# Kernel tuning notes

Measured on AMD Instinct MI355X. Metric: run time of the kernel, lower is better.

The kernel has to match this reference:

```python
import jax, jax.numpy as jnp
import numpy as np

B, N, DIM = 4, 2048, 128
HEADS, HEAD = 8, 128
INNER = HEADS * HEAD  # 1024
EPS = 1e-5


def setup_inputs() -> dict:
    key = jax.random.key(0)
    k0, k1, k2 = jax.random.split(key, 3)
    return {
        "x": jax.random.normal(k0, (B, N, DIM), jnp.float32),
        "ln_gamma": jnp.ones((DIM,), jnp.float32),
        "ln_beta": jnp.zeros((DIM,), jnp.float32),
        "w_qkv": jax.random.normal(k1, (3 * INNER, DIM), jnp.float32) * (DIM ** -0.5),
        "w_out": jax.random.normal(k2, (DIM, INNER), jnp.float32) * (INNER ** -0.5),
        "b_out": jnp.zeros((DIM,), jnp.float32),
    }


def _rope(t):
    """lucidrains-style rotary embedding over full last dim of t: [b,h,n,d]."""
    n, d = t.shape[-2], t.shape[-1]
    inv_freq = 1.0 / (10000.0 ** (jnp.arange(0, d, 2, dtype=jnp.float32) / d))
    freqs = jnp.arange(n, dtype=jnp.float32)[:, None] * inv_freq[None, :]  # [n, d/2]
    freqs = jnp.repeat(freqs, 2, axis=-1)  # interleaved duplicate -> [n, d]
    cos, sin = jnp.cos(freqs), jnp.sin(freqs)
    # rotate_half on interleaved pairs: (x1, x2) -> (-x2, x1)
    x1, x2 = t[..., 0::2], t[..., 1::2]
    rot = jnp.stack((-x2, x1), axis=-1).reshape(t.shape)
    return t * cos + rot * sin


def reference(x, ln_gamma, ln_beta, w_qkv, w_out, b_out):
    # LayerNorm
    mu = x.mean(-1, keepdims=True)
    var = x.var(-1, keepdims=True)
    xn = (x - mu) * jax.lax.rsqrt(var + EPS) * ln_gamma + ln_beta
    # QKV projection (bias-free)
    qkv = jnp.einsum('bnd,ed->bne', xn, w_qkv)  # [B, N, 3*INNER]
    q, k, v = jnp.split(qkv, 3, axis=-1)
    to_heads = lambda t: t.reshape(B, N, HEADS, HEAD).transpose(0, 2, 1, 3)
    q, k, v = to_heads(q), to_heads(k), to_heads(v)  # [B, H, N, HEAD]
    # Partial RoPE: rotate all but the last token; last token stays unrotated
    q = jnp.concatenate([_rope(q[:, :, :-1]), q[:, :, -1:]], axis=2)
    k = jnp.concatenate([_rope(k[:, :, :-1]), k[:, :, -1:]], axis=2)
    scale = HEAD ** -0.5
    dots = jnp.einsum('bhid,bhjd->bhij', q, k) * scale  # [B, H, N, N]
    attn = jax.nn.softmax(dots, axis=-1)
    out = jnp.einsum('bhij,bhjd->bhid', attn, v)
    out = out.transpose(0, 2, 1, 3).reshape(B, N, INNER)
    return out @ w_out.T + b_out
```

## Files before the change

kernel.cpp:

```cpp
#include <hip/hip_runtime.h>
#include <hip/hip_bf16.h>
#include <hip/hip_fp16.h>

#define B_      4
#define N_      2048
#define DIM_    128
#define HEADS_  8
#define HEAD_   128
#define INNER_  1024
#define QKV_    3072
#define EPS_    1e-5f
#define SCALE_  0.08838834764831845f
#define ROPE_C  0.20762050593046015f

typedef __attribute__((ext_vector_type(8))) short short8;
typedef __attribute__((ext_vector_type(4))) short short4v;
typedef __attribute__((ext_vector_type(4))) float f32x4;
typedef __attribute__((ext_vector_type(16))) float f32x16;


__device__ __forceinline__ unsigned short f2bf(float f) {
    unsigned u = __builtin_bit_cast(unsigned, f);
    u = (u + 0x7fffu + ((u >> 16) & 1u)) >> 16;
    return (unsigned short)u;
}
__device__ __forceinline__ float bf2f(unsigned short h) {
    unsigned u = ((unsigned)h) << 16;
    return __builtin_bit_cast(float, u);
}
__device__ __forceinline__ unsigned pk2(float a, float b) {
    return (unsigned)f2bf(a) | ((unsigned)f2bf(b) << 16);
}
__device__ __forceinline__ short4v pack4(const float* e) {
    __hip_bfloat162 h0 = __float22bfloat162_rn(make_float2(e[0], e[1]));
    __hip_bfloat162 h1 = __float22bfloat162_rn(make_float2(e[2], e[3]));
    uint2 u;
    __builtin_memcpy(&u.x, &h0, 4);
    __builtin_memcpy(&u.y, &h1, 4);
    return __builtin_bit_cast(short4v, u);
}

__global__ __launch_bounds__(256) void k_prep(
    const float* __restrict__ x, const float* __restrict__ g,
    const float* __restrict__ be, const float* __restrict__ w_qkv,
    const float* __restrict__ w_out, unsigned short* __restrict__ xnb,
    unsigned short* __restrict__ wqb, unsigned short* __restrict__ wob)
{
    const int bid = blockIdx.x;
    if (bid < 2048) {
        const int w = threadIdx.x >> 6, l = threadIdx.x & 63;
        const int row = bid * 4 + w;
        float2 v = *(const float2*)(x + (size_t)row * 128 + l * 2);
        float s = v.x + v.y, s2 = v.x * v.x + v.y * v.y;
#pragma unroll
        for (int off = 1; off < 64; off <<= 1) {
            s  += __shfl_xor(s, off);
            s2 += __shfl_xor(s2, off);
        }
        float mu = s * (1.f / 128.f);
        float var = s2 * (1.f / 128.f) - mu * mu;
        float rs = rsqrtf(var + EPS_);
        float2 gg = *(const float2*)(g + l * 2);
        float2 bb = *(const float2*)(be + l * 2);
        float ox = (v.x - mu) * rs * gg.x + bb.x;
        float oy = (v.y - mu) * rs * gg.y + bb.y;
        *(unsigned*)(xnb + (size_t)row * 128 + l * 2) = pk2(ox, oy);
    } else if (bid < 2240) {
        size_t i = ((size_t)(bid - 2048) * 256 + threadIdx.x) * 8;
        float4 f0 = *(const float4*)(w_qkv + i), f1 = *(const float4*)(w_qkv + i + 4);
        uint4 u = { pk2(f0.x, f0.y), pk2(f0.z, f0.w), pk2(f1.x, f1.y), pk2(f1.z, f1.w) };
        *(uint4*)(wqb + i) = u;
    } else {
        size_t i = ((size_t)(bid - 2240) * 256 + threadIdx.x) * 8;
        float4 f0 = *(const float4*)(w_out + i), f1 = *(const float4*)(w_out + i + 4);
        uint4 u = { pk2(f0.x, f0.y), pk2(f0.z, f0.w), pk2(f1.x, f1.y), pk2(f1.z, f1.w) };
        *(uint4*)(wob + i) = u;
    }
}

__global__ __launch_bounds__(256) void k_qkvf(
    const unsigned short* __restrict__ xnb, const unsigned short* __restrict__ wb,
    unsigned short* __restrict__ Q, unsigned short* __restrict__ K,
    unsigned short* __restrict__ Vt)
{
    __shared__ unsigned short lA[128 * 128];
    __shared__ unsigned short lB[128 * 128];
    const int t = threadIdx.x;
    const int wv = t >> 6, l = t & 63;
    const int lm = l & 15, quad = l >> 4;
    const int row0 = blockIdx.x * 128;
    const int by   = blockIdx.y;
    const int e0   = by * 128;

#pragma unroll
    for (int i = 0; i < 8; ++i) {
        int c = t + 256 * i;  int r = c >> 4, c8 = c & 15;
        int sc = (c8 ^ (r & 7)) * 8;
        *(uint4*)&lA[r * 128 + sc] =
            *(const uint4*)(xnb + (size_t)(row0 + r) * 128 + c8 * 8);
        *(uint4*)&lB[r * 128 + sc] =
            *(const uint4*)(wb + (size_t)(e0 + r) * 128 + c8 * 8);
    }
    __syncthreads();

    short8 af[2][4];
#pragma unroll
    for (int mt = 0; mt < 2; ++mt)
#pragma unroll
        for (int ks = 0; ks < 4; ++ks) {
            int r = wv * 32 + mt * 16 + lm;
            af[mt][ks] = *(short8*)&lA[r * 128 + (((ks * 4 + quad) ^ (r & 7)) << 3)];
        }

    f32x4 acc[2][8];
#pragma unroll
    for (int mt = 0; mt < 2; ++mt)
#pragma unroll
        for (int ct = 0; ct < 8; ++ct) acc[mt][ct] = (f32x4){0.f, 0.f, 0.f, 0.f};
#pragma unroll
    for (int ks = 0; ks < 4; ++ks) {
#pragma unroll
        for (int ct = 0; ct < 8; ++ct) {
            int r = ct * 16 + lm;
            short8 b = *(short8*)&lB[r * 128 + (((ks * 4 + quad) ^ (r & 7)) << 3)];
            acc[0][ct] = __builtin_amdgcn_mfma_f32_16x16x32_bf16(af[0][ks], b, acc[0][ct], 0, 0, 0);
            acc[1][ct] = __builtin_amdgcn_mfma_f32_16x16x32_bf16(af[1][ks], b, acc[1][ct], 0, 0, 0);
        }
    }
    __syncthreads();

    const int b  = row0 >> 11;
    const int n0 = row0 & (N_ - 1);
    const int h  = by & 7;
    const int bh = b * 8 + h;

    if (by < 16) {
#pragma unroll
        for (int mt = 0; mt < 2; ++mt)
#pragma unroll
            for (int ct = 0; ct < 8; ++ct)
#pragma unroll
                for (int r = 0; r < 4; ++r) {
                    int row = wv * 32 + mt * 16 + quad * 4 + r;
                    int chunk = ct * 2 + (lm >> 3);
                    lA[row * 128 + ((chunk ^ (row & 7)) << 3) + (lm & 7)] =
                        f2bf(acc[mt][ct][r]);
                }
        __syncthreads();

        const int r_loc = t >> 1, half = t & 1;
        const int n = n0 + r_loc;
        unsigned short* dst = (by < 8 ? Q : K) +
            ((size_t)bh * N_ + n) * HEAD_ + half * 64;
        const bool dorope = (n != N_ - 1);
#pragma unroll
        for (int j = 0; j < 8; ++j) {
            short8 vv = *(short8*)&lA[r_loc * 128 + (((half * 8 + j) ^ (r_loc & 7)) << 3)];
            if (dorope) {
                unsigned short* pv = (unsigned short*)&vv;
#pragma unroll
                for (int p = 0; p < 4; ++p) {
                    int i0 = half * 32 + j * 4 + p;
                    float invf = exp2f(-(float)i0 * ROPE_C);
                    float th = (float)n * invf;
                    float cs = __cosf(th), sn = __sinf(th);
                    float e = bf2f(pv[2 * p]), o = bf2f(pv[2 * p + 1]);
                    pv[2 * p]     = f2bf(e * cs - o * sn);
                    pv[2 * p + 1] = f2bf(o * cs + e * sn);
                }
            }
            *(short8*)(dst + j * 8) = vv;
        }
    } else {
#pragma unroll
        for (int mt = 0; mt < 2; ++mt)
#pragma unroll
            for (int ct = 0; ct < 8; ++ct)
#pragma unroll
                for (int r = 0; r < 4; ++r) {
                    int row = ct * 16 + lm;
                    int chunk = wv * 4 + mt * 2 + (quad & 1);
                    int off   = (quad >> 1) * 4 + r;
                    lA[row * 128 + ((chunk ^ (row & 7)) << 3) + off] =
                        f2bf(acc[mt][ct][r]);
                }
        __syncthreads();

        const int d = t >> 1, half = t & 1;
        unsigned short* dst = Vt + ((size_t)bh * HEAD_ + d) * N_ + n0 + half * 64;
#pragma unroll
        for (int j = 0; j < 8; ++j)
            *(short8*)(dst + j * 8) =
                *(short8*)&lA[d * 128 + (((half * 8 + j) ^ (d & 7)) << 3)];
    }
}

__global__ __launch_bounds__(256) void k_attn(
    const unsigned short* __restrict__ Q, const unsigned short* __restrict__ K,
    const unsigned short* __restrict__ Vt, unsigned short* __restrict__ Ob)
{
    __shared__ unsigned short lK[64 * 136];
    __shared__ unsigned short lV[128 * 72];

    const int t = threadIdx.x;
    const int w = t >> 6, l = t & 63;
    const int q32 = l & 31, hi = l >> 5;
    const int bid = blockIdx.x;
    const int bh = bid & 31;
    const int qt = bid >> 5;
    const int n0 = qt * 128;
    const unsigned short* Qb = Q  + (size_t)bh * N_ * HEAD_;
    const unsigned short* Kb = K  + (size_t)bh * N_ * HEAD_;
    const unsigned short* Vb = Vt + (size_t)bh * N_ * HEAD_;

    short8 aq[8];
    {
        const unsigned short* qp =
            Qb + (size_t)(n0 + w * 32 + q32) * 128 + hi * 8;
#pragma unroll
        for (int kc = 0; kc < 8; ++kc)
            aq[kc] = *(const short8*)(qp + kc * 16);
    }

    f32x16 Oa[4];
#pragma unroll
    for (int i = 0; i < 4; ++i)
        Oa[i] = (f32x16){0.f,0.f,0.f,0.f,0.f,0.f,0.f,0.f,
                         0.f,0.f,0.f,0.f,0.f,0.f,0.f,0.f};
    float ps = 0.f;
    const float C1 = SCALE_ * 1.44269504f;
    const float C0 = -23.08312f;

    short8 kr[4], vr[4];
#pragma unroll
    for (int i = 0; i < 4; ++i) {
        int c = t + 256 * i;
        kr[i] = *(const short8*)(Kb + ((size_t)(c >> 4)) * 128 + (c & 15) * 8);
        vr[i] = *(const short8*)(Vb + (size_t)(c >> 3) * N_ + (c & 7) * 8);
    }

    for (int jt = 0; jt < 32; ++jt) {
        __syncthreads();
#pragma unroll
        for (int i = 0; i < 4; ++i) {
            int c = t + 256 * i;
            *(short8*)&lK[(c >> 4) * 136 + (c & 15) * 8] = kr[i];
            *(short8*)&lV[(c >> 3) * 72  + (c & 7)  * 8] = vr[i];
        }
        __syncthreads();
        if (jt < 31) {
#pragma unroll
            for (int i = 0; i < 4; ++i) {
                int c = t + 256 * i;
                kr[i] = *(const short8*)(Kb + ((size_t)((jt + 1) * 64 + (c >> 4))) * 128 + (c & 15) * 8);
                vr[i] = *(const short8*)(Vb + (size_t)(c >> 3) * N_ + (jt + 1) * 64 + (c & 7) * 8);
            }
        }

        f32x16 st0 = (f32x16){0.f,0.f,0.f,0.f,0.f,0.f,0.f,0.f,
                              0.f,0.f,0.f,0.f,0.f,0.f,0.f,0.f};
        f32x16 st1 = st0;
#pragma unroll
        for (int kc = 0; kc < 8; ++kc) {
            short8 kf0 = *(short8*)&lK[q32 * 136 + kc * 16 + hi * 8];
            short8 kf1 = *(short8*)&lK[(32 + q32) * 136 + kc * 16 + hi * 8];
            st0 = __builtin_amdgcn_mfma_f32_32x32x16_bf16(kf0, aq[kc], st0, 0, 0, 0);
            st1 = __builtin_amdgcn_mfma_f32_32x32x16_bf16(kf1, aq[kc], st1, 0, 0, 0);
        }

        short8 pa[4];
#pragma unroll
        for (int T = 0; T < 2; ++T) {
#pragma unroll
            for (int g = 0; g < 2; ++g) {
                float e[8];
#pragma unroll
                for (int j = 0; j < 8; ++j) {
                    float s = T ? st1[8 * g + j] : st0[8 * g + j];
                    e[j] = exp2f(s * C1 + C0);
                    ps += e[j];
                }
                short4v lo = pack4(e);
                short4v hh = pack4(e + 4);
                pa[T * 2 + g] = __builtin_shufflevector(lo, hh, 0, 1, 2, 3, 4, 5, 6, 7);
            }
        }

#pragma unroll
        for (int dt = 0; dt < 4; ++dt) {
            const int d = dt * 32 + q32;
#pragma unroll
            for (int kc = 0; kc < 4; ++kc) {
                short8 bv = *(short8*)&lV[d * 72 + kc * 16 + hi * 8];
                Oa[dt] = __builtin_amdgcn_mfma_f32_32x32x16_bf16(pa[kc], bv, Oa[dt], 0, 0, 0);
            }
        }
    }

    ps += __shfl_xor(ps, 32);
    float inv = 1.f / ps;
    float ilq[16];
#pragma unroll
    for (int m = 0; m < 4; ++m)
#pragma unroll
        for (int r = 0; r < 4; ++r)
            ilq[m * 4 + r] = __shfl(inv, 4 * hi + r + 8 * m);

    const int b = bh >> 3, h = bh & 7;
#pragma unroll
    for (int dt = 0; dt < 4; ++dt) {
        const int d = dt * 32 + q32;
#pragma unroll
        for (int m = 0; m < 4; ++m)
#pragma unroll
            for (int r = 0; r < 4; ++r) {
                int q = 4 * hi + r + 8 * m;
                int n = n0 + w * 32 + q;
                Ob[((size_t)b * N_ + n) * INNER_ + h * HEAD_ + d] =
                    f2bf(Oa[dt][m * 4 + r] * ilq[m * 4 + r]);
            }
    }
}

__global__ __launch_bounds__(256) void k_proj(
    const unsigned short* __restrict__ Ob, const unsigned short* __restrict__ wob,
    const float* __restrict__ bias, float* __restrict__ out)
{
    __shared__ unsigned short lA[32 * 136];
    __shared__ unsigned short lB[64 * 136];
    float* lCf = (float*)lA;
    const int t = threadIdx.x;
    const int wv = t >> 6, l = t & 63;
    const int lm = l & 15, quad = l >> 4;
    const int rt = wv & 1, ch = wv >> 1;
    const int row0 = blockIdx.x * 32;
    const int e0   = blockIdx.y * 64;

    f32x4 acc[2];
#pragma unroll
    for (int ct = 0; ct < 2; ++ct) acc[ct] = (f32x4){0.f, 0.f, 0.f, 0.f};

    for (int kt = 0; kt < 8; ++kt) {
        __syncthreads();
#pragma unroll
        for (int i = 0; i < 2; ++i) {
            int c = t + 256 * i;  int r = c >> 4, c8 = c & 15;
            *(uint4*)&lA[r * 136 + c8 * 8] =
                *(const uint4*)(Ob + (size_t)(row0 + r) * 1024 + kt * 128 + c8 * 8);
        }
#pragma unroll
        for (int i = 0; i < 4; ++i) {
            int c = t + 256 * i;  int r = c >> 4, c8 = c & 15;
            *(uint4*)&lB[r * 136 + c8 * 8] =
                *(const uint4*)(wob + (size_t)(e0 + r) * 1024 + kt * 128 + c8 * 8);
        }
        __syncthreads();
        short8 a_[4];
#pragma unroll
        for (int ks = 0; ks < 4; ++ks)
            a_[ks] = *(short8*)&lA[(rt * 16 + lm) * 136 + ks * 32 + quad * 8];
#pragma unroll
        for (int ks = 0; ks < 4; ++ks)
#pragma unroll
            for (int ct = 0; ct < 2; ++ct) {
                short8 b = *(short8*)&lB[(ch * 32 + ct * 16 + lm) * 136 + ks * 32 + quad * 8];
                acc[ct] = __builtin_amdgcn_mfma_f32_16x16x32_bf16(a_[ks], b, acc[ct], 0, 0, 0);
            }
    }
    __syncthreads();
#pragma unroll
    for (int ct = 0; ct < 2; ++ct)
#pragma unroll
        for (int r = 0; r < 4; ++r)
            lCf[(rt * 16 + quad * 4 + r) * 68 + ch * 32 + ct * 16 + lm] = acc[ct][r];
    __syncthreads();
#pragma unroll
    for (int i = 0; i < 2; ++i) {
        int c = t + 256 * i;  int r = c >> 4, c4 = c & 15;
        float4 v = *(float4*)&lCf[r * 68 + c4 * 4];
        float4 b4 = *(const float4*)(bias + e0 + c4 * 4);
        v.x += b4.x; v.y += b4.y; v.z += b4.z; v.w += b4.w;
        *(float4*)(out + (size_t)(row0 + r) * 128 + e0 + c4 * 4) = v;
    }
}

extern "C" void kernel_launch(void* const* d_in, const int* in_sizes, int n_in,
                              void* d_out, int out_size, void* d_ws, size_t ws_size,
                              hipStream_t stream) {
    const float* x      = (const float*)d_in[0];
    const float* gamma  = (const float*)d_in[1];
    const float* beta   = (const float*)d_in[2];
    const float* w_qkv  = (const float*)d_in[3];
    const float* w_out  = (const float*)d_in[4];
    const float* b_out  = (const float*)d_in[5];
    float* out = (float*)d_out;
    char* wsb = (char*)d_ws;
    unsigned short* Q    = (unsigned short*)(wsb);
    unsigned short* K    = (unsigned short*)(wsb + (16ull << 20));
    unsigned short* Vt   = (unsigned short*)(wsb + (32ull << 20));
    unsigned short* Ob   = (unsigned short*)(wsb + (48ull << 20));
    unsigned short* xnb  = (unsigned short*)(wsb + (96ull << 20));
    unsigned short* wqb  = (unsigned short*)(wsb + (98ull << 20));
    unsigned short* wob  = (unsigned short*)(wsb + (99ull << 20));

    k_prep <<<dim3(2304),    256, 0, stream>>>(x, gamma, beta, w_qkv, w_out,
                                               xnb, wqb, wob);
    k_qkvf <<<dim3(64, 24),  256, 0, stream>>>(xnb, wqb, Q, K, Vt);
    k_attn <<<dim3(512),     256, 0, stream>>>(Q, K, Vt, Ob);
    k_proj <<<dim3(256, 2),  256, 0, stream>>>(Ob, wob, b_out, out);
}
```

Before: 191.2 us.

## Fuse output projection into attention kernel via per-head atomic accumulation

Removes the separate projection kernel and the bf16 intermediate attention-output buffer. Each attention block stages its normalized output tile in shared memory, multiplies it by the matching head slice of the output weight using MFMA, and atomically adds the partial sums into the fp32 output. The prep kernel now initializes the output with the bias. This saves one launch plus a global write and read of the intermediate, but adds 8-way atomic contention per output element and makes the summation order nondeterministic.

```diff
diff --git a/kernel.cpp b/kernel.cpp
--- a/kernel.cpp
+++ b/kernel.cpp
@@ -43,8 +43,9 @@
 __global__ __launch_bounds__(256) void k_prep(
     const float* __restrict__ x, const float* __restrict__ g,
     const float* __restrict__ be, const float* __restrict__ w_qkv,
-    const float* __restrict__ w_out, unsigned short* __restrict__ xnb,
-    unsigned short* __restrict__ wqb, unsigned short* __restrict__ wob)
+    const float* __restrict__ w_out, const float* __restrict__ bias,
+    unsigned short* __restrict__ xnb, unsigned short* __restrict__ wqb,
+    unsigned short* __restrict__ wob, float* __restrict__ out)
 {
     const int bid = blockIdx.x;
     if (bid < 2048) {
@@ -70,11 +71,15 @@
         float4 f0 = *(const float4*)(w_qkv + i), f1 = *(const float4*)(w_qkv + i + 4);
         uint4 u = { pk2(f0.x, f0.y), pk2(f0.z, f0.w), pk2(f1.x, f1.y), pk2(f1.z, f1.w) };
         *(uint4*)(wqb + i) = u;
-    } else {
+    } else if (bid < 2304) {
         size_t i = ((size_t)(bid - 2240) * 256 + threadIdx.x) * 8;
         float4 f0 = *(const float4*)(w_out + i), f1 = *(const float4*)(w_out + i + 4);
         uint4 u = { pk2(f0.x, f0.y), pk2(f0.z, f0.w), pk2(f1.x, f1.y), pk2(f1.z, f1.w) };
         *(uint4*)(wob + i) = u;
+    } else {
+        size_t i = ((size_t)(bid - 2304) * 256 + threadIdx.x) * 4;
+        float4 bb = *(const float4*)(bias + (i & 127));
+        *(float4*)(out + i) = bb;
     }
 }
 
@@ -197,10 +202,12 @@
 
 __global__ __launch_bounds__(256) void k_attn(
     const unsigned short* __restrict__ Q, const unsigned short* __restrict__ K,
-    const unsigned short* __restrict__ Vt, unsigned short* __restrict__ Ob)
+    const unsigned short* __restrict__ Vt, const unsigned short* __restrict__ wob,
+    float* __restrict__ out)
 {
-    __shared__ unsigned short lK[64 * 136];
-    __shared__ unsigned short lV[128 * 72];
+    __shared__ unsigned short pool[64 * 136 + 128 * 72];
+    unsigned short* lK = pool;
+    unsigned short* lV = pool + 64 * 136;
 
     const int t = threadIdx.x;
     const int w = t >> 6, l = t & 63;
@@ -306,7 +313,8 @@
         for (int r = 0; r < 4; ++r)
             ilq[m * 4 + r] = __shfl(inv, 4 * hi + r + 8 * m);
 
-    const int b = bh >> 3, h = bh & 7;
+    __syncthreads();
+    unsigned short* Ot = pool + w * 4352;
 #pragma unroll
     for (int dt = 0; dt < 4; ++dt) {
         const int d = dt * 32 + q32;
@@ -314,73 +322,38 @@
         for (int m = 0; m < 4; ++m)
 #pragma unroll
             for (int r = 0; r < 4; ++r) {
-                int q = 4 * hi + r + 8 * m;
-                int n = n0 + w * 32 + q;
-                Ob[((size_t)b * N_ + n) * INNER_ + h * HEAD_ + d] =
-                    f2bf(Oa[dt][m * 4 + r] * ilq[m * 4 + r]);
-            }
-    }
-}
-
-__global__ __launch_bounds__(256) void k_proj(
-    const unsigned short* __restrict__ Ob, const unsigned short* __restrict__ wob,
-    const float* __restrict__ bias, float* __restrict__ out)
-{
-    __shared__ unsigned short lA[32 * 136];
-    __shared__ unsigned short lB[64 * 136];
-    float* lCf = (float*)lA;
-    const int t = threadIdx.x;
-    const int wv = t >> 6, l = t & 63;
-    const int lm = l & 15, quad = l >> 4;
-    const int rt = wv & 1, ch = wv >> 1;
-    const int row0 = blockIdx.x * 32;
-    const int e0   = blockIdx.y * 64;
-
-    f32x4 acc[2];
-#pragma unroll
-    for (int ct = 0; ct < 2; ++ct) acc[ct] = (f32x4){0.f, 0.f, 0.f, 0.f};
-
-    for (int kt = 0; kt < 8; ++kt) {
-        __syncthreads();
-#pragma unroll
-        for (int i = 0; i < 2; ++i) {
-            int c = t + 256 * i;  int r = c >> 4, c8 = c & 15;
-            *(uint4*)&lA[r * 136 + c8 * 8] =
-                *(const uint4*)(Ob + (size_t)(row0 + r) * 1024 + kt * 128 + c8 * 8);
-        }
-#pragma unroll
-        for (int i = 0; i < 4; ++i) {
-            int c = t + 256 * i;  int r = c >> 4, c8 = c & 15;
-            *(uint4*)&lB[r * 136 + c8 * 8] =
-                *(const uint4*)(wob + (size_t)(e0 + r) * 1024 + kt * 128 + c8 * 8);
-        }
-        __syncthreads();
-        short8 a_[4];
-#pragma unroll
-        for (int ks = 0; ks < 4; ++ks)
-            a_[ks] = *(short8*)&lA[(rt * 16 + lm) * 136 + ks * 32 + quad * 8];
-#pragma unroll
-        for (int ks = 0; ks < 4; ++ks)
-#pragma unroll
-            for (int ct = 0; ct < 2; ++ct) {
-                short8 b = *(short8*)&lB[(ch * 32 + ct * 16 + lm) * 136 + ks * 32 + quad * 8];
-                acc[ct] = __builtin_amdgcn_mfma_f32_16x16x32_bf16(a_[ks], b, acc[ct], 0, 0, 0);
+                int ql = 4 * hi + r + 8 * m;
+                Ot[ql * 136 + d] = f2bf(Oa[dt][m * 4 + r] * ilq[m * 4 + r]);
             }
     }
     __syncthreads();
-#pragma unroll
-    for (int ct = 0; ct < 2; ++ct)
-#pragma unroll
-        for (int r = 0; r < 4; ++r)
-            lCf[(rt * 16 + quad * 4 + r) * 68 + ch * 32 + ct * 16 + lm] = acc[ct][r];
-    __syncthreads();
-#pragma unroll
-    for (int i = 0; i < 2; ++i) {
-        int c = t + 256 * i;  int r = c >> 4, c4 = c & 15;
-        float4 v = *(float4*)&lCf[r * 68 + c4 * 4];
-        float4 b4 = *(const float4*)(bias + e0 + c4 * 4);
-        v.x += b4.x; v.y += b4.y; v.z += b4.z; v.w += b4.w;
-        *(float4*)(out + (size_t)(row0 + r) * 128 + e0 + c4 * 4) = v;
+
+    short8 aO[8];
+#pragma unroll
+    for (int kc = 0; kc < 8; ++kc)
+        aO[kc] = *(short8*)&Ot[q32 * 136 + kc * 16 + hi * 8];
+
+    const int b = bh >> 3, h = bh & 7;
+    float* outB = out + ((size_t)b * N_ + n0 + w * 32) * 128;
+
+#pragma unroll
+    for (int et = 0; et < 4; ++et) {
+        f32x16 pc = (f32x16){0.f,0.f,0.f,0.f,0.f,0.f,0.f,0.f,
+                             0.f,0.f,0.f,0.f,0.f,0.f,0.f,0.f};
+#pragma unroll
+        for (int kc = 0; kc < 8; ++kc) {
+            short8 wB = *(const short8*)(
+                wob + (size_t)(et * 32 + q32) * 1024 + h * 128 + kc * 16 + hi * 8);
+            pc = __builtin_amdgcn_mfma_f32_32x32x16_bf16(aO[kc], wB, pc, 0, 0, 0);
+        }
+#pragma unroll
+        for (int m = 0; m < 4; ++m)
+#pragma unroll
+            for (int r = 0; r < 4; ++r) {
+                int ql = 4 * hi + r + 8 * m;
+                unsafeAtomicAdd(outB + (size_t)ql * 128 + et * 32 + q32,
+                                pc[m * 4 + r]);
+            }
     }
 }
 
@@ -398,14 +371,12 @@
     unsigned short* Q    = (unsigned short*)(wsb);
     unsigned short* K    = (unsigned short*)(wsb + (16ull << 20));
     unsigned short* Vt   = (unsigned short*)(wsb + (32ull << 20));
-    unsigned short* Ob   = (unsigned short*)(wsb + (48ull << 20));
     unsigned short* xnb  = (unsigned short*)(wsb + (96ull << 20));
     unsigned short* wqb  = (unsigned short*)(wsb + (98ull << 20));
     unsigned short* wob  = (unsigned short*)(wsb + (99ull << 20));
 
-    k_prep <<<dim3(2304),    256, 0, stream>>>(x, gamma, beta, w_qkv, w_out,
-                                               xnb, wqb, wob);
+    k_prep <<<dim3(3328),    256, 0, stream>>>(x, gamma, beta, w_qkv, w_out,
+                                               b_out, xnb, wqb, wob, out);
     k_qkvf <<<dim3(64, 24),  256, 0, stream>>>(xnb, wqb, Q, K, Vt);
-    k_attn <<<dim3(512),     256, 0, stream>>>(Q, K, Vt, Ob);
-    k_proj <<<dim3(256, 2),  256, 0, stream>>>(Ob, wob, b_out, out);
-}
+    k_attn <<<dim3(512),     256, 0, stream>>>(Q, K, Vt, wob, out);
+}
```

Result: slower. 196.7 us (+2.8%).
